# Kernel optimization log

Hardware: AMD Instinct MI355X
Metric: run time of the kernel (lower is better)

The kernel has to match this reference:

```python
import jax, jax.numpy as jnp
import numpy as np

DIM = 1024
N_HEADS = 16
HEAD_DIM = DIM // N_HEADS


def setup_inputs() -> dict:
    key = jax.random.key(0)
    ks = jax.random.split(key, 7)
    s = 1.0 / np.sqrt(DIM)
    return {
        "hidden_states": jax.random.normal(ks[0], (1, 4096, DIM), dtype=jnp.float32),
        "Wq": jax.random.uniform(ks[1], (DIM, DIM), jnp.float32, -s, s),
        "bq": jax.random.uniform(ks[2], (DIM,), jnp.float32, -s, s),
        "Wk": jax.random.uniform(ks[3], (DIM, DIM), jnp.float32, -s, s),
        "bk": jax.random.uniform(ks[4], (DIM,), jnp.float32, -s, s),
        "Wv": jax.random.uniform(ks[5], (DIM, DIM), jnp.float32, -s, s),
        "bv": jax.random.uniform(ks[6], (DIM,), jnp.float32, -s, s),
    }


def _split_heads(x):
    # [B, S, DIM] -> [B, H, S, HEAD_DIM]
    b, s, _ = x.shape
    return x.reshape(b, s, N_HEADS, HEAD_DIM).transpose(0, 2, 1, 3)


def reference(hidden_states, Wq, bq, Wk, bk, Wv, bv):
    q = _split_heads(hidden_states @ Wq + bq)
    k = _split_heads(hidden_states @ Wk + bk)
    v = _split_heads(hidden_states @ Wv + bv)
    scores = jnp.einsum("bhqd,bhkd->bhqk", q, k) / np.sqrt(HEAD_DIM).astype(np.float32)
    probs = jax.nn.softmax(scores, axis=-1)  # dropout prob = 0 -> identity
    ctx = jnp.einsum("bhqk,bhkd->bhqd", probs, v)
    b, h, s, d = ctx.shape
    return ctx.transpose(0, 2, 1, 3).reshape(b, s, h * d)
```

## Files before the change

### kernel.cpp

```cpp
#include <hip/hip_runtime.h>
#include <hip/hip_bf16.h>

#define S_LEN 4096
#define DIM   1024
#define NH    16
#define HD    64

typedef unsigned short u16;
typedef short  bf16x8 __attribute__((ext_vector_type(8)));
typedef float  f32x4  __attribute__((ext_vector_type(4)));

__device__ __forceinline__ u16 f2bf(float f){
  union { float f; unsigned u; } x; x.f = f;
  unsigned u = x.u;
  return (u16)((u + 0x7FFFu + ((u >> 16) & 1u)) >> 16);
}
__device__ __forceinline__ unsigned pk2(float a, float b){
  union { __hip_bfloat162 h; unsigned u; } x;
  x.h = __float22bfloat162_rn(float2{a, b});
  return x.u;
}
__device__ __forceinline__ void ld2lds16(const u16* g, u16* l){
  __builtin_amdgcn_global_load_lds((const __attribute__((address_space(1))) void*)g,
                                   (__attribute__((address_space(3))) void*)l, 16, 0, 0);
}

#define QSCALE 0.1803368801111204f

__global__ __launch_bounds__(256) void fill_sentinel(float* __restrict__ out, int n){
  int i = blockIdx.x * 256 + threadIdx.x;
  if (i < n) out[i] = 77.0f;
}

__global__ __launch_bounds__(256) void conv_x(const float* __restrict__ X, u16* __restrict__ Xb){
  size_t i = ((size_t)blockIdx.x * 256 + threadIdx.x) * 8;
  float4 v0 = *(const float4*)(X + i);
  float4 v1 = *(const float4*)(X + i + 4);
  uint4 w;
  w.x = pk2(v0.x, v0.y); w.y = pk2(v0.z, v0.w);
  w.z = pk2(v1.x, v1.y); w.w = pk2(v1.z, v1.w);
  *(uint4*)(Xb + i) = w;
}

__global__ __launch_bounds__(256) void transpose_w(
    const float* __restrict__ W0, const float* __restrict__ W1, const float* __restrict__ W2,
    u16* __restrict__ Wt)
{
  const float* W = blockIdx.z==0 ? W0 : blockIdx.z==1 ? W1 : W2;
  u16* T = Wt + (size_t)blockIdx.z * DIM * DIM;
  __shared__ __align__(16) u16 tile[64*72];
  int k0 = blockIdx.x*64, n0 = blockIdx.y*64;
  int t = threadIdx.x;
  #pragma unroll
  for (int i = 0; i < 4; ++i){
    int idx = t + i*256;
    int row = idx >> 4, col4 = (idx & 15) * 4;
    float4 v = *(const float4*)(W + (size_t)(k0+row)*DIM + n0 + col4);
    tile[(col4+0)*72 + row] = f2bf(v.x);
    tile[(col4+1)*72 + row] = f2bf(v.y);
    tile[(col4+2)*72 + row] = f2bf(v.z);
    tile[(col4+3)*72 + row] = f2bf(v.w);
  }
  __syncthreads();
  #pragma unroll
  for (int i = 0; i < 2; ++i){
    int idx = t + i*256;
    int n = idx >> 3, k16 = (idx & 7) * 8;
    *(int4*)(T + (size_t)(n0+n)*DIM + k0 + k16) = *(const int4*)(tile + n*72 + k16);
  }
}

__device__ __forceinline__ void qkv_epilogue(
    int z, int m0, int n0, int wm, int wn, int quad, int l15,
    const f32x4 acc[4][4], const float* bias,
    u16* __restrict__ qb, u16* __restrict__ kf_out, u16* __restrict__ vf_out)
{
  #pragma unroll
  for (int nt=0; nt<4; ++nt){
    int n = n0 + wn + nt*16 + l15;
    float bv = bias[n];
    int h = n >> 6, d = n & 63;
    #pragma unroll
    for (int mt=0; mt<4; ++mt){
      int mb = m0 + wm + mt*16 + quad*4;
      f32x4 c = acc[mt][nt];
      if (z == 0){
        #pragma unroll
        for (int r=0; r<4; ++r)
          qb[(size_t)(mb + r)*DIM + n] = f2bf((c[r] + bv) * QSCALE);
      } else if (z == 1){
        int half = d >> 5, quadk = (d >> 3) & 3, j = d & 7;
        #pragma unroll
        for (int r=0; r<4; ++r){
          int s = mb + r;
          size_t idx = ((((size_t)h*256 + (s >> 4))*2 + half)*64 + quadk*16 + (s & 15))*8 + j;
          kf_out[idx] = f2bf(c[r] + bv);
        }
      } else {
        int kt64 = mb >> 6, c2 = (mb >> 5) & 1, quadv = (mb >> 3) & 3, j0 = mb & 7;
        int dt = d >> 4, l15v = d & 15;
        size_t base = (((((size_t)h*64 + kt64)*4 + dt)*2 + c2)*64 + quadv*16 + l15v)*8 + j0;
        ushort4 p;
        p.x = f2bf(c[0]+bv); p.y = f2bf(c[1]+bv);
        p.z = f2bf(c[2]+bv); p.w = f2bf(c[3]+bv);
        *(ushort4*)(vf_out + base) = p;
      }
    }
  }
}

__global__ __launch_bounds__(256) void qkv_gemm_fast(
    const u16* __restrict__ Xbf, const u16* __restrict__ Wt,
    const float* __restrict__ b0, const float* __restrict__ b1, const float* __restrict__ b2,
    u16* __restrict__ qb, u16* __restrict__ kf_out, u16* __restrict__ vf_out)
{
  int z = blockIdx.z;
  const u16* Wz = Wt + (size_t)z * DIM * DIM;
  const float* bias = z==0 ? b0 : z==1 ? b1 : b2;

  __shared__ __align__(16) u16 As[128*32];
  __shared__ __align__(16) u16 Bs[128*32];

  int m0 = blockIdx.x * 128, n0 = blockIdx.y * 128;
  int t = threadIdx.x, wave = t >> 6, lane = t & 63, quad = lane >> 4, l15 = lane & 15;
  int wm = (wave >> 1) * 64, wn = (wave & 1) * 64;

  f32x4 acc[4][4];
  #pragma unroll
  for (int i=0;i<4;++i)
    #pragma unroll
    for (int j=0;j<4;++j) acc[i][j] = (f32x4){0.f,0.f,0.f,0.f};

  int srow = wave*32 + (lane >> 2);
  int skc  = (lane & 3) * 8;
  const u16* gA0 = Xbf + (size_t)(m0 + srow)*DIM + skc;
  const u16* gA1 = gA0 + (size_t)16*DIM;
  const u16* gB0 = Wz  + (size_t)(n0 + srow)*DIM + skc;
  const u16* gB1 = gB0 + (size_t)16*DIM;
  u16* lA0 = As + srow*32 + skc;
  u16* lA1 = lA0 + 16*32;
  u16* lB0 = Bs + srow*32 + skc;
  u16* lB1 = lB0 + 16*32;

  for (int kt = 0; kt < 32; ++kt){
    int ko = kt * 32;
    __syncthreads();
    ld2lds16(gA0 + ko, lA0);
    ld2lds16(gA1 + ko, lA1);
    ld2lds16(gB0 + ko, lB0);
    ld2lds16(gB1 + ko, lB1);
    __syncthreads();
    bf16x8 af[4], bfr[4];
    #pragma unroll
    for (int mt=0; mt<4; ++mt) af[mt]  = *(const bf16x8*)(As + (wm + mt*16 + l15)*32 + quad*8);
    #pragma unroll
    for (int nt=0; nt<4; ++nt) bfr[nt] = *(const bf16x8*)(Bs + (wn + nt*16 + l15)*32 + quad*8);
    #pragma unroll
    for (int mt=0; mt<4; ++mt)
      #pragma unroll
      for (int nt=0; nt<4; ++nt)
        acc[mt][nt] = __builtin_amdgcn_mfma_f32_16x16x32_bf16(af[mt], bfr[nt], acc[mt][nt], 0, 0, 0);
  }
  qkv_epilogue(z, m0, n0, wm, wn, quad, l15, acc, bias, qb, kf_out, vf_out);
}

__global__ __launch_bounds__(256) void qkv_gemm_legacy(
    const float* __restrict__ X,
    const float* __restrict__ Wq, const float* __restrict__ Wk, const float* __restrict__ Wv,
    const float* __restrict__ b0, const float* __restrict__ b1, const float* __restrict__ b2,
    u16* __restrict__ qb, u16* __restrict__ kf_out, u16* __restrict__ vf_out)
{
  int z = blockIdx.z;
  const float* W    = z==0 ? Wq : z==1 ? Wk : Wv;
  const float* bias = z==0 ? b0 : z==1 ? b1 : b2;

  __shared__ __align__(16) u16 As[128*40];
  __shared__ __align__(16) u16 Bs[128*40];

  int m0 = blockIdx.x * 128, n0 = blockIdx.y * 128;
  int t = threadIdx.x, wave = t >> 6, lane = t & 63, quad = lane >> 4, l15 = lane & 15;
  int wm = (wave >> 1) * 64, wn = (wave & 1) * 64;

  f32x4 acc[4][4];
  #pragma unroll
  for (int i=0;i<4;++i)
    #pragma unroll
    for (int j=0;j<4;++j) acc[i][j] = (f32x4){0.f,0.f,0.f,0.f};

  int sr = t >> 2, sc = (t & 3) * 8;
  const float* gA0 = X + (size_t)(m0 + sr) * DIM + sc;
  const float* gA1 = X + (size_t)(m0 + 64 + sr) * DIM + sc;
  int br = t >> 3, bc = (t & 7) * 16;
  const float* gW = W + (size_t)br * DIM + n0 + bc;

  for (int kt = 0; kt < 32; ++kt){
    int ko = kt * 32;
    float4 a00 = *(const float4*)(gA0 + ko);
    float4 a01 = *(const float4*)(gA0 + ko + 4);
    float4 a10 = *(const float4*)(gA1 + ko);
    float4 a11 = *(const float4*)(gA1 + ko + 4);
    float4 w0  = *(const float4*)(gW + (size_t)ko*DIM);
    float4 w1  = *(const float4*)(gW + (size_t)ko*DIM + 4);
    float4 w2  = *(const float4*)(gW + (size_t)ko*DIM + 8);
    float4 w3  = *(const float4*)(gW + (size_t)ko*DIM + 12);
    int4 pa0, pa1;
    pa0.x = pk2(a00.x,a00.y); pa0.y = pk2(a00.z,a00.w);
    pa0.z = pk2(a01.x,a01.y); pa0.w = pk2(a01.z,a01.w);
    pa1.x = pk2(a10.x,a10.y); pa1.y = pk2(a10.z,a10.w);
    pa1.z = pk2(a11.x,a11.y); pa1.w = pk2(a11.z,a11.w);
    u16 wb[16];
    wb[0]=f2bf(w0.x); wb[1]=f2bf(w0.y); wb[2]=f2bf(w0.z); wb[3]=f2bf(w0.w);
    wb[4]=f2bf(w1.x); wb[5]=f2bf(w1.y); wb[6]=f2bf(w1.z); wb[7]=f2bf(w1.w);
    wb[8]=f2bf(w2.x); wb[9]=f2bf(w2.y); wb[10]=f2bf(w2.z); wb[11]=f2bf(w2.w);
    wb[12]=f2bf(w3.x); wb[13]=f2bf(w3.y); wb[14]=f2bf(w3.z); wb[15]=f2bf(w3.w);
    __syncthreads();
    *(int4*)(As + sr*40 + sc)      = pa0;
    *(int4*)(As + (64+sr)*40 + sc) = pa1;
    #pragma unroll
    for (int j=0;j<16;++j) Bs[(bc+j)*40 + br] = wb[j];
    __syncthreads();
    bf16x8 af[4], bfr[4];
    #pragma unroll
    for (int mt=0; mt<4; ++mt) af[mt]  = *(const bf16x8*)(As + (wm + mt*16 + l15)*40 + quad*8);
    #pragma unroll
    for (int nt=0; nt<4; ++nt) bfr[nt] = *(const bf16x8*)(Bs + (wn + nt*16 + l15)*40 + quad*8);
    #pragma unroll
    for (int mt=0; mt<4; ++mt)
      #pragma unroll
      for (int nt=0; nt<4; ++nt)
        acc[mt][nt] = __builtin_amdgcn_mfma_f32_16x16x32_bf16(af[mt], bfr[nt], acc[mt][nt], 0, 0, 0);
  }
  qkv_epilogue(z, m0, n0, wm, wn, quad, l15, acc, bias, qb, kf_out, vf_out);
}

#define PSTR 72
__global__ __launch_bounds__(256, 2) void attn(
    const u16* __restrict__ Qb, const u16* __restrict__ Kf,
    const u16* __restrict__ Vf, float* __restrict__ out)
{
  int h = blockIdx.y;
  int t = threadIdx.x, wave = t >> 6, lane = t & 63, quad = lane >> 4, l15 = lane & 15;
  int q0 = blockIdx.x * 128 + wave * 32;

  __shared__ __align__(16) u16 Ps[4*16*PSTR];
  u16* Pw = Ps + wave * (16*PSTR);

  const u16* Kfh = Kf + (size_t)h * 262144;
  const u16* Vfh = Vf + (size_t)h * 262144;

  bf16x8 qf[2][2];
  #pragma unroll
  for (int qs=0; qs<2; ++qs){
    const u16* Qp = Qb + (size_t)(q0 + qs*16 + l15)*DIM + h*HD;
    qf[qs][0] = *(const bf16x8*)(Qp + quad*8);
    qf[qs][1] = *(const bf16x8*)(Qp + 32 + quad*8);
  }

  f32x4 O[2][4];
  #pragma unroll
  for (int qs=0; qs<2; ++qs)
    #pragma unroll
    for (int dt=0; dt<4; ++dt) O[qs][dt] = (f32x4){0.f,0.f,0.f,0.f};
  float lsum[2] = {0.f, 0.f};

  for (int kt = 0; kt < 64; ++kt){
    bf16x8 kfr[4][2];
    #pragma unroll
    for (int kn=0; kn<4; ++kn)
      #pragma unroll
      for (int hf=0; hf<2; ++hf)
        kfr[kn][hf] = *(const bf16x8*)(Kfh + ((((size_t)kt*4 + kn)*2 + hf)*64 + lane)*8);
    bf16x8 vfr[4][2];
    #pragma unroll
    for (int dt=0; dt<4; ++dt)
      #pragma unroll
      for (int c2=0; c2<2; ++c2)
        vfr[dt][c2] = *(const bf16x8*)(Vfh + ((((size_t)kt*4 + dt)*2 + c2)*64 + lane)*8);

    #pragma unroll
    for (int qs=0; qs<2; ++qs){
      f32x4 st[4];
      #pragma unroll
      for (int kn=0; kn<4; ++kn){
        f32x4 zz = (f32x4){0.f,0.f,0.f,0.f};
        zz = __builtin_amdgcn_mfma_f32_16x16x32_bf16(kfr[kn][0], qf[qs][0], zz, 0,0,0);
        zz = __builtin_amdgcn_mfma_f32_16x16x32_bf16(kfr[kn][1], qf[qs][1], zz, 0,0,0);
        st[kn] = zz;
      }
      float ls = 0.f;
      #pragma unroll
      for (int kn=0; kn<4; ++kn)
        #pragma unroll
        for (int r=0; r<4; ++r){
          float p = __builtin_amdgcn_exp2f(st[kn][r]);
          st[kn][r] = p;
          ls += p;
        }
      lsum[qs] += ls;
      __builtin_amdgcn_wave_barrier();
      #pragma unroll
      for (int kn=0; kn<4; ++kn){
        uint2 w;
        w.x = pk2(st[kn][0], st[kn][1]);
        w.y = pk2(st[kn][2], st[kn][3]);
        *(uint2*)(Pw + l15*PSTR + kn*16 + quad*4) = w;
      }
      __builtin_amdgcn_wave_barrier();
      bf16x8 pf0 = *(const bf16x8*)(Pw + l15*PSTR + quad*8);
      bf16x8 pf1 = *(const bf16x8*)(Pw + l15*PSTR + 32 + quad*8);
      __builtin_amdgcn_wave_barrier();
      #pragma unroll
      for (int dt=0; dt<4; ++dt){
        f32x4 o = O[qs][dt];
        o = __builtin_amdgcn_mfma_f32_16x16x32_bf16(vfr[dt][0], pf0, o, 0,0,0);
        o = __builtin_amdgcn_mfma_f32_16x16x32_bf16(vfr[dt][1], pf1, o, 0,0,0);
        O[qs][dt] = o;
      }
    }
  }
  #pragma unroll
  for (int qs=0; qs<2; ++qs){
    float l = lsum[qs];
    l += __shfl_xor(l, 16, 64);
    l += __shfl_xor(l, 32, 64);
    float inv = 1.0f / l;
    int query = q0 + qs*16 + l15;
    #pragma unroll
    for (int dt=0; dt<4; ++dt){
      float4 v;
      v.x = O[qs][dt][0]*inv; v.y = O[qs][dt][1]*inv;
      v.z = O[qs][dt][2]*inv; v.w = O[qs][dt][3]*inv;
      *(float4*)(out + (size_t)query*DIM + h*HD + dt*16 + quad*4) = v;
    }
  }
}

extern "C" void kernel_launch(void* const* d_in, const int* in_sizes, int n_in,
                              void* d_out, int out_size, void* d_ws, size_t ws_size,
                              hipStream_t stream)
{
  const float* X  = (const float*)d_in[0];
  const float* Wq = (const float*)d_in[1];
  const float* bq = (const float*)d_in[2];
  const float* Wk = (const float*)d_in[3];
  const float* bk = (const float*)d_in[4];
  const float* Wv = (const float*)d_in[5];
  const float* bv = (const float*)d_in[6];
  float* out = (float*)d_out;
  u16*   ws  = (u16*)d_ws;

  const size_t SD = (size_t)S_LEN * DIM;
  const size_t need_fast = (4*SD + 3*(size_t)DIM*DIM) * sizeof(u16);
  const size_t need_min  = (size_t)24 * 1024 * 1024;

  if (ws_size >= need_fast){
    u16* xbf = ws;
    u16* wt  = xbf + SD;
    u16* qb  = wt + 3*(size_t)DIM*DIM;
    u16* kf  = qb + SD;
    u16* vf  = kf + SD;
    conv_x       <<<dim3((int)(SD/8/256)), 256, 0, stream>>>(X, xbf);
    transpose_w  <<<dim3(16,16,3), 256, 0, stream>>>(Wq, Wk, Wv, wt);
    qkv_gemm_fast<<<dim3(32, 8, 3), 256, 0, stream>>>(xbf, wt, bq, bk, bv, qb, kf, vf);
    attn         <<<dim3(32, 16   ), 256, 0, stream>>>(qb, kf, vf, out);
  } else if (ws_size >= need_min){
    u16* qb = ws;
    u16* kf = qb + SD;
    u16* vf = kf + SD;
    qkv_gemm_legacy<<<dim3(32, 8, 3), 256, 0, stream>>>(X, Wq, Wk, Wv, bq, bk, bv, qb, kf, vf);
    attn           <<<dim3(32, 16   ), 256, 0, stream>>>(qb, kf, vf, out);
  } else {
    fill_sentinel<<<(out_size + 255)/256, 256, 0, stream>>>(out, out_size);
  }
}
```

Baseline: 215.4 us.

## Double-buffer K fragments in registers and ping-pong P tiles in attention loop

The attention main loop now prefetches the next key tile's fragments into a second register set while computing the current one, unrolled by two with alternating register buffers. Both query subtiles' QK^T products are issued together. P is written to per-subtile LDS slots, with separate slots for even and odd iterations, which removes most wave barriers between write and read. The goal is to hide global-load latency for K and give the scheduler more independent MFMA work, at the cost of higher register pressure and four times the LDS for P.

```diff
diff --git a/kernel.cpp b/kernel.cpp
--- a/kernel.cpp
+++ b/kernel.cpp
@@ -234,6 +234,7 @@
 }
 
 #define PSTR 72
+#define PQS  (16*PSTR)
 __global__ __launch_bounds__(256, 2) void attn(
     const u16* __restrict__ Qb, const u16* __restrict__ Kf,
     const u16* __restrict__ Vf, float* __restrict__ out)
@@ -242,8 +243,8 @@
   int t = threadIdx.x, wave = t >> 6, lane = t & 63, quad = lane >> 4, l15 = lane & 15;
   int q0 = blockIdx.x * 128 + wave * 32;
 
-  __shared__ __align__(16) u16 Ps[4*16*PSTR];
-  u16* Pw = Ps + wave * (16*PSTR);
+  __shared__ __align__(16) u16 Ps[4*4*PQS];
+  u16* Pw = Ps + wave * (4*PQS);
 
   const u16* Kfh = Kf + (size_t)h * 262144;
   const u16* Vfh = Vf + (size_t)h * 262144;
@@ -263,61 +264,91 @@
     for (int dt=0; dt<4; ++dt) O[qs][dt] = (f32x4){0.f,0.f,0.f,0.f};
   float lsum[2] = {0.f, 0.f};
 
-  for (int kt = 0; kt < 64; ++kt){
-    bf16x8 kfr[4][2];
-    #pragma unroll
-    for (int kn=0; kn<4; ++kn)
-      #pragma unroll
-      for (int hf=0; hf<2; ++hf)
-        kfr[kn][hf] = *(const bf16x8*)(Kfh + ((((size_t)kt*4 + kn)*2 + hf)*64 + lane)*8);
-    bf16x8 vfr[4][2];
-    #pragma unroll
-    for (int dt=0; dt<4; ++dt)
-      #pragma unroll
-      for (int c2=0; c2<2; ++c2)
-        vfr[dt][c2] = *(const bf16x8*)(Vfh + ((((size_t)kt*4 + dt)*2 + c2)*64 + lane)*8);
-
-    #pragma unroll
-    for (int qs=0; qs<2; ++qs){
-      f32x4 st[4];
-      #pragma unroll
-      for (int kn=0; kn<4; ++kn){
-        f32x4 zz = (f32x4){0.f,0.f,0.f,0.f};
-        zz = __builtin_amdgcn_mfma_f32_16x16x32_bf16(kfr[kn][0], qf[qs][0], zz, 0,0,0);
-        zz = __builtin_amdgcn_mfma_f32_16x16x32_bf16(kfr[kn][1], qf[qs][1], zz, 0,0,0);
-        st[kn] = zz;
-      }
-      float ls = 0.f;
+  const u16* kbase = Kfh + (size_t)lane*8;
+  const u16* vbase = Vfh + (size_t)lane*8;
+
+#define ATTN_BODY(KBUF, KTV, PPAR)                                               \
+  do {                                                                           \
+    bf16x8 vfr[4][2];                                                            \
+    const u16* vb = vbase + (size_t)(KTV)*4096;                                  \
+    _Pragma("unroll")                                                            \
+    for (int dt=0; dt<4; ++dt)                                                   \
+      _Pragma("unroll")                                                          \
+      for (int c2=0; c2<2; ++c2)                                                 \
+        vfr[dt][c2] = *(const bf16x8*)(vb + (dt*2+c2)*512);                      \
+    f32x4 st[2][4];                                                              \
+    _Pragma("unroll")                                                            \
+    for (int qs=0; qs<2; ++qs)                                                   \
+      _Pragma("unroll")                                                          \
+      for (int kn=0; kn<4; ++kn){                                                \
+        f32x4 zz = (f32x4){0.f,0.f,0.f,0.f};                                     \
+        zz = __builtin_amdgcn_mfma_f32_16x16x32_bf16(KBUF[kn][0], qf[qs][0], zz, 0,0,0); \
+        zz = __builtin_amdgcn_mfma_f32_16x16x32_bf16(KBUF[kn][1], qf[qs][1], zz, 0,0,0); \
+        st[qs][kn] = zz;                                                         \
+      }                                                                          \
+    _Pragma("unroll")                                                            \
+    for (int qs=0; qs<2; ++qs){                                                  \
+      float ls = 0.f;                                                            \
+      u16* Pq = (PPAR) + qs*PQS;                                                 \
+      _Pragma("unroll")                                                          \
+      for (int kn=0; kn<4; ++kn){                                                \
+        _Pragma("unroll")                                                        \
+        for (int r=0; r<4; ++r){                                                 \
+          float p = __builtin_amdgcn_exp2f(st[qs][kn][r]);                       \
+          st[qs][kn][r] = p; ls += p;                                            \
+        }                                                                        \
+        uint2 w;                                                                 \
+        w.x = pk2(st[qs][kn][0], st[qs][kn][1]);                                 \
+        w.y = pk2(st[qs][kn][2], st[qs][kn][3]);                                 \
+        *(uint2*)(Pq + l15*PSTR + kn*16 + quad*4) = w;                           \
+      }                                                                          \
+      lsum[qs] += ls;                                                            \
+    }                                                                            \
+    __builtin_amdgcn_wave_barrier();                                             \
+    _Pragma("unroll")                                                            \
+    for (int qs=0; qs<2; ++qs){                                                  \
+      const u16* Pq = (PPAR) + qs*PQS;                                           \
+      bf16x8 pf0 = *(const bf16x8*)(Pq + l15*PSTR + quad*8);                     \
+      bf16x8 pf1 = *(const bf16x8*)(Pq + l15*PSTR + 32 + quad*8);                \
+      _Pragma("unroll")                                                          \
+      for (int dt=0; dt<4; ++dt){                                                \
+        f32x4 o = O[qs][dt];                                                     \
+        o = __builtin_amdgcn_mfma_f32_16x16x32_bf16(vfr[dt][0], pf0, o, 0,0,0);  \
+        o = __builtin_amdgcn_mfma_f32_16x16x32_bf16(vfr[dt][1], pf1, o, 0,0,0);  \
+        O[qs][dt] = o;                                                           \
+      }                                                                          \
+    }                                                                            \
+  } while(0)
+
+  bf16x8 KA[4][2], KB[4][2];
+  #pragma unroll
+  for (int kn=0; kn<4; ++kn)
+    #pragma unroll
+    for (int hf=0; hf<2; ++hf)
+      KA[kn][hf] = *(const bf16x8*)(kbase + (kn*2+hf)*512);
+
+  for (int kt = 0; kt < 64; kt += 2){
+    {
+      const u16* kb1 = kbase + (size_t)(kt+1)*4096;
       #pragma unroll
       for (int kn=0; kn<4; ++kn)
         #pragma unroll
-        for (int r=0; r<4; ++r){
-          float p = __builtin_amdgcn_exp2f(st[kn][r]);
-          st[kn][r] = p;
-          ls += p;
-        }
-      lsum[qs] += ls;
-      __builtin_amdgcn_wave_barrier();
+        for (int hf=0; hf<2; ++hf)
+          KB[kn][hf] = *(const bf16x8*)(kb1 + (kn*2+hf)*512);
+      ATTN_BODY(KA, kt, Pw);
+    }
+    {
+      const u16* kb2 = kbase + (size_t)((kt+2)&63)*4096;
       #pragma unroll
-      for (int kn=0; kn<4; ++kn){
-        uint2 w;
-        w.x = pk2(st[kn][0], st[kn][1]);
-        w.y = pk2(st[kn][2], st[kn][3]);
-        *(uint2*)(Pw + l15*PSTR + kn*16 + quad*4) = w;
-      }
-      __builtin_amdgcn_wave_barrier();
-      bf16x8 pf0 = *(const bf16x8*)(Pw + l15*PSTR + quad*8);
-      bf16x8 pf1 = *(const bf16x8*)(Pw + l15*PSTR + 32 + quad*8);
-      __builtin_amdgcn_wave_barrier();
-      #pragma unroll
-      for (int dt=0; dt<4; ++dt){
-        f32x4 o = O[qs][dt];
-        o = __builtin_amdgcn_mfma_f32_16x16x32_bf16(vfr[dt][0], pf0, o, 0,0,0);
-        o = __builtin_amdgcn_mfma_f32_16x16x32_bf16(vfr[dt][1], pf1, o, 0,0,0);
-        O[qs][dt] = o;
-      }
+      for (int kn=0; kn<4; ++kn)
+        #pragma unroll
+        for (int hf=0; hf<2; ++hf)
+          KA[kn][hf] = *(const bf16x8*)(kb2 + (kn*2+hf)*512);
+      ATTN_BODY(KB, kt+1, Pw + 2*PQS);
     }
   }
+#undef ATTN_BODY
+
   #pragma unroll
   for (int qs=0; qs<2; ++qs){
     float l = lsum[qs];
```

Measured after the change: 213.0 us. Within noise of the previous version (-1.1%).
